# Optimization experiments

Hardware: AMD Instinct MI355X
Metric: run time of the kernel (lower is better)

## Reference

```python
import jax, jax.numpy as jnp
import numpy as np
from math import log2, ceil

HEADS, DIM_HEAD, BLOCK, EPS = 16, 64, 16, 1e-8


def setup_inputs() -> dict:
    key = jax.random.key(0)
    k1, k2, k3, k4 = jax.random.split(key, 4)
    b, n, dim = 4, 4096, 1024
    inner = HEADS * DIM_HEAD
    return {
        "x": jax.random.normal(k1, (b, n, dim), jnp.float32),
        "w_qkv": jax.random.normal(k2, (inner * 3, dim), jnp.float32) * 0.02,
        "w_out": jax.random.normal(k3, (dim, inner), jnp.float32) * 0.02,
        "b_out": jax.random.normal(k4, (dim,), jnp.float32) * 0.02,
    }


def reference(x, w_qkv, w_out, b_out):
    b, n, dim = x.shape
    pad_to_len = 2 ** ceil(log2(n))
    if pad_to_len != n:
        x = jnp.pad(x, ((0, 0), (0, pad_to_len - n), (0, 0)))
    qkv = x @ w_qkv.T  # torch Linear (no bias): weight is [out, in]
    q, k, v = jnp.split(qkv, 3, axis=-1)

    def split_heads(t):
        return t.reshape(b, pad_to_len, HEADS, DIM_HEAD).transpose(0, 2, 1, 3).reshape(b * HEADS, pad_to_len, DIM_HEAD)

    q = split_heads(q) * DIM_HEAD ** -0.5
    k = split_heads(k)
    v = split_heads(v)

    num_levels = int(log2(pad_to_len // BLOCK)) - 1
    # hierarchical coarsening: q,k averaged over pairs, v summed over pairs
    qkvs = [(q, k, v)]
    for _ in range(num_levels):
        q = q.reshape(q.shape[0], -1, 2, DIM_HEAD).mean(2)
        k = k.reshape(k.shape[0], -1, 2, DIM_HEAD).mean(2)
        v = v.reshape(v.shape[0], -1, 2, DIM_HEAD).sum(2)
        qkvs.append((q, k, v))

    neg_max = -jnp.finfo(x.dtype).max
    idx = jnp.arange(pad_to_len)
    Ysum = jnp.zeros((b * HEADS, pad_to_len, DIM_HEAD), x.dtype)
    Asum = jnp.zeros((b * HEADS, pad_to_len), x.dtype)

    for lvl, (ql, kl, vl) in enumerate(qkvs):
        B = ql.shape[0]
        nb = ql.shape[1] // BLOCK  # number of blocks at this level
        ql = ql.reshape(B, nb, BLOCK, DIM_HEAD)
        kl = kl.reshape(B, nb, BLOCK, DIM_HEAD)
        vl = vl.reshape(B, nb, BLOCK, DIM_HEAD)
        if lvl == 0:
            # finest level: causal diagonal block attention
            S = jnp.einsum('bnid,bnjd->bnij', ql, kl)
            S = jnp.where(jnp.triu(jnp.ones((BLOCK, BLOCK), bool), 1), neg_max, S)
            S = S - S.max(-1, keepdims=True)
            A = jnp.exp(S)
            y = jnp.einsum('bnij,bnjd->bnid', A, vl).reshape(B, pad_to_len, DIM_HEAD)
            Av = A.sum(-1).reshape(B, pad_to_len)
        else:
            # off-diagonal: second block of each pair attends to first block of pair
            q2 = ql.reshape(B, nb // 2, 2, BLOCK, DIM_HEAD)[:, :, 1]
            k1b = kl.reshape(B, nb // 2, 2, BLOCK, DIM_HEAD)[:, :, 0]  # flip_every_two then take [:,1]
            v1b = vl.reshape(B, nb // 2, 2, BLOCK, DIM_HEAD)[:, :, 0]
            S = jnp.einsum('bnid,bnjd->bnij', q2, k1b)
            S = S - S.max(-1, keepdims=True)
            A = jnp.exp(S)
            y = jnp.einsum('bnij,bnjd->bnid', A, v1b)  # [B, nb/2, BLOCK, d]
            Av = A.sum(-1)
            # zero-pad first block of each pair, flatten blocks back to sequence
            y = jnp.pad(y[:, :, None], ((0, 0), (0, 0), (1, 0), (0, 0), (0, 0))).reshape(B, -1, DIM_HEAD)
            Av = jnp.pad(Av[:, :, None], ((0, 0), (0, 0), (1, 0), (0, 0))).reshape(B, -1)
            # expand coarsened positions to full resolution (consecutive repeats)
            y = jnp.repeat(y, 2 ** lvl, axis=1)
            Av = jnp.repeat(Av, 2 ** lvl, axis=1)
        # causal keep-mask: max original index inside the coarsened key group <= query index
        seq_key = (idx >> lvl << lvl) + (2 ** lvl - 1)
        keep = seq_key <= idx  # at lvl=0 seq_key == idx -> keep all
        Ysum = Ysum + jnp.where(keep[None, :, None], y, 0.0)
        Asum = Asum + jnp.where(keep[None, :], Av, 0.0)

    out = Ysum / (Asum + EPS)[..., None]
    out = out.reshape(b, HEADS, pad_to_len, DIM_HEAD).transpose(0, 2, 1, 3).reshape(b, pad_to_len, HEADS * DIM_HEAD)
    out = out @ w_out.T + b_out
    return out[:, :n]
```

## Files before the change

kernel.cpp:

```cpp
#include <hip/hip_runtime.h>

typedef __bf16 bf16_t;
typedef __attribute__((ext_vector_type(8))) __bf16 bf16x8;
typedef __attribute__((ext_vector_type(4))) float f32x4;

#define MFMA(a,b,c) __builtin_amdgcn_mfma_f32_16x16x32_bf16(a,b,c,0,0,0)

static __device__ __forceinline__ unsigned short f2bfbits(float f){
  unsigned int u = __builtin_bit_cast(unsigned int, f);
  return (unsigned short)((u + 0x7FFFu + ((u >> 16) & 1u)) >> 16);
}
static __device__ __forceinline__ float bits2f(unsigned int b){
  return __builtin_bit_cast(float, b << 16);
}
static __device__ __forceinline__ void gl_lds16(const void* g, void* l){
  __builtin_amdgcn_global_load_lds(
      (const __attribute__((address_space(1))) void*)(g),
      (__attribute__((address_space(3))) void*)(l), 16, 0, 0);
}
static __device__ __forceinline__ void unpack8(uint4 raw, float* f){
  f[0]=bits2f(raw.x&0xFFFFu); f[1]=bits2f(raw.x>>16);
  f[2]=bits2f(raw.y&0xFFFFu); f[3]=bits2f(raw.y>>16);
  f[4]=bits2f(raw.z&0xFFFFu); f[5]=bits2f(raw.z>>16);
  f[6]=bits2f(raw.w&0xFFFFu); f[7]=bits2f(raw.w>>16);
}

__global__ __launch_bounds__(256) void cvt_f32_bf16(const float* __restrict__ in,
                                                    unsigned short* __restrict__ out,
                                                    long n4){
  const long stride = (long)gridDim.x * 256;
  for (long i = (long)blockIdx.x * 256 + threadIdx.x; i < n4; i += stride){
    float4 v = *(const float4*)(in + i * 4);
    unsigned long long pack = (unsigned long long)f2bfbits(v.x)
      | ((unsigned long long)f2bfbits(v.y) << 16)
      | ((unsigned long long)f2bfbits(v.z) << 32)
      | ((unsigned long long)f2bfbits(v.w) << 48);
    *(unsigned long long*)(out + i * 4) = pack;
  }
}

template<int MODE>
__global__ __launch_bounds__(512, 2) void gemm256(
    const unsigned short* __restrict__ A, const unsigned short* __restrict__ B,
    const int K, const int nbx,
    unsigned short* __restrict__ oq, unsigned short* __restrict__ ok2, unsigned short* __restrict__ ov,
    float* __restrict__ outp, const float* __restrict__ bias)
{
  __shared__ char lds[131072];
  const int t = threadIdx.x;
  const int lane = t & 63, wid = t >> 6;
  const int wr = wid >> 2, wc = wid & 3;
  const int r16 = lane & 15, g = lane >> 4;

  const int nb = gridDim.x, cpx = nb >> 3;
  const int lin = (blockIdx.x & 7) * cpx + (blockIdx.x >> 3);
  const int by = lin / nbx, bx = lin - by * nbx;
  const long row0 = (long)by * 256, col0 = (long)bx * 256;

  const unsigned short* gA[4]; const unsigned short* gB[4];
  int ldsoff[4];
  #pragma unroll
  for (int r2 = 0; r2 < 4; ++r2){
    const int flat = r2*512 + t;
    const int row = flat >> 3, slot = flat & 7;
    const int slotg = slot ^ (row & 7);
    gA[r2] = A + (row0 + row) * K + slotg*8;
    gB[r2] = B + (col0 + row) * K + slotg*8;
    ldsoff[r2] = (r2*512 + wid*64) * 16;
  }

  f32x4 acc[8][4];
  #pragma unroll
  for (int m = 0; m < 8; ++m)
    #pragma unroll
    for (int n = 0; n < 4; ++n)
      acc[m][n] = (f32x4){0.f, 0.f, 0.f, 0.f};

  const int nk = K >> 6;

  #define SA(tt, r) gl_lds16(gA[r] + (tt)*64, lds + ((tt)&1)*65536 + ldsoff[r])
  #define SB(tt, r) gl_lds16(gB[r] + (tt)*64, lds + ((tt)&1)*65536 + 32768 + ldsoff[r])

  SA(0,0); SA(0,2); SB(0,0); SB(0,1); SB(0,2); SB(0,3); SA(0,1); SA(0,3);
  asm volatile("s_waitcnt vmcnt(2)" ::: "memory");
  __builtin_amdgcn_s_barrier();

  for (int kt = 0; kt < nk; ++kt){
    char* ldsA = lds + (kt & 1)*65536;
    char* ldsB = ldsA + 32768;
    const bool more = (kt + 1 < nk);
    bf16x8 bfrag[4][2];

    {
      #pragma unroll
      for (int n = 0; n < 4; ++n)
        #pragma unroll
        for (int kk = 0; kk < 2; ++kk){
          const int row = wc*64 + n*16 + r16;
          bfrag[n][kk] = *(const bf16x8*)(ldsB + row*128 + (((kk*4 + g) ^ (row & 7)) * 16));
        }
      bf16x8 afr[2][2];
      #pragma unroll
      for (int mi = 0; mi < 2; ++mi)
        #pragma unroll
        for (int kk = 0; kk < 2; ++kk){
          const int row = wr*128 + mi*16 + r16;
          afr[mi][kk] = *(const bf16x8*)(ldsA + row*128 + (((kk*4 + g) ^ (row & 7)) * 16));
        }
      if (more){ SA(kt+1,0); SA(kt+1,2); }
      __builtin_amdgcn_s_barrier();
      asm volatile("s_waitcnt lgkmcnt(0)" ::: "memory");
      __builtin_amdgcn_sched_barrier(0);
      __builtin_amdgcn_s_setprio(1);
      #pragma unroll
      for (int mi = 0; mi < 2; ++mi)
        #pragma unroll
        for (int n = 0; n < 4; ++n)
          #pragma unroll
          for (int kk = 0; kk < 2; ++kk)
            acc[mi][n] = MFMA(afr[mi][kk], bfrag[n][kk], acc[mi][n]);
      __builtin_amdgcn_s_setprio(0);
      __builtin_amdgcn_s_barrier();
    }
    {
      bf16x8 afr[2][2];
      #pragma unroll
      for (int mi = 0; mi < 2; ++mi)
        #pragma unroll
        for (int kk = 0; kk < 2; ++kk){
          const int row = wr*128 + (2+mi)*16 + r16;
          afr[mi][kk] = *(const bf16x8*)(ldsA + row*128 + (((kk*4 + g) ^ (row & 7)) * 16));
        }
      if (more){
        SB(kt+1,0); SB(kt+1,1);
        asm volatile("s_waitcnt vmcnt(4)" ::: "memory");
      } else {
        asm volatile("s_waitcnt vmcnt(0)" ::: "memory");
      }
      __builtin_amdgcn_s_barrier();
      asm volatile("s_waitcnt lgkmcnt(0)" ::: "memory");
      __builtin_amdgcn_sched_barrier(0);
      __builtin_amdgcn_s_setprio(1);
      #pragma unroll
      for (int mi = 0; mi < 2; ++mi)
        #pragma unroll
        for (int n = 0; n < 4; ++n)
          #pragma unroll
          for (int kk = 0; kk < 2; ++kk)
            acc[2+mi][n] = MFMA(afr[mi][kk], bfrag[n][kk], acc[2+mi][n]);
      __builtin_amdgcn_s_setprio(0);
      __builtin_amdgcn_s_barrier();
    }
    {
      bf16x8 afr[2][2];
      #pragma unroll
      for (int mi = 0; mi < 2; ++mi)
        #pragma unroll
        for (int kk = 0; kk < 2; ++kk){
          const int row = wr*128 + (4+mi)*16 + r16;
          afr[mi][kk] = *(const bf16x8*)(ldsA + row*128 + (((kk*4 + g) ^ (row & 7)) * 16));
        }
      if (more){ SB(kt+1,2); SB(kt+1,3); }
      __builtin_amdgcn_s_barrier();
      asm volatile("s_waitcnt lgkmcnt(0)" ::: "memory");
      __builtin_amdgcn_sched_barrier(0);
      __builtin_amdgcn_s_setprio(1);
      #pragma unroll
      for (int mi = 0; mi < 2; ++mi)
        #pragma unroll
        for (int n = 0; n < 4; ++n)
          #pragma unroll
          for (int kk = 0; kk < 2; ++kk)
            acc[4+mi][n] = MFMA(afr[mi][kk], bfrag[n][kk], acc[4+mi][n]);
      __builtin_amdgcn_s_setprio(0);
      __builtin_amdgcn_s_barrier();
    }
    {
      bf16x8 afr[2][2];
      #pragma unroll
      for (int mi = 0; mi < 2; ++mi)
        #pragma unroll
        for (int kk = 0; kk < 2; ++kk){
          const int row = wr*128 + (6+mi)*16 + r16;
          afr[mi][kk] = *(const bf16x8*)(ldsA + row*128 + (((kk*4 + g) ^ (row & 7)) * 16));
        }
      if (more){
        SA(kt+1,1); SA(kt+1,3);
        asm volatile("s_waitcnt vmcnt(2)" ::: "memory");
      }
      __builtin_amdgcn_s_barrier();
      asm volatile("s_waitcnt lgkmcnt(0)" ::: "memory");
      __builtin_amdgcn_sched_barrier(0);
      __builtin_amdgcn_s_setprio(1);
      #pragma unroll
      for (int mi = 0; mi < 2; ++mi)
        #pragma unroll
        for (int n = 0; n < 4; ++n)
          #pragma unroll
          for (int kk = 0; kk < 2; ++kk)
            acc[6+mi][n] = MFMA(afr[mi][kk], bfrag[n][kk], acc[6+mi][n]);
      __builtin_amdgcn_s_setprio(0);
      __builtin_amdgcn_s_barrier();
    }
  }
  #undef SA
  #undef SB

  if (MODE == 0){
    __syncthreads();
    const int which = (int)(col0 >> 10);
    const int h = (int)((col0 & 1023) >> 6) + wc;
    const float sc = (which == 0) ? 0.125f : 1.0f;
    unsigned short* st = (unsigned short*)lds + wid*8192;
    #pragma unroll
    for (int pass = 0; pass < 2; ++pass){
      #pragma unroll
      for (int mm = 0; mm < 4; ++mm)
        #pragma unroll
        for (int n = 0; n < 4; ++n)
          #pragma unroll
          for (int q2 = 0; q2 < 4; ++q2)
            st[(mm*16 + g*4 + q2)*72 + n*16 + r16] = f2bfbits(acc[pass*4 + mm][n][q2] * sc);
      const long prow0 = row0 + wr*128 + pass*64;
      if (which < 2){
        unsigned short* dst = (which == 0) ? oq : ok2;
        #pragma unroll
        for (int rd = 0; rd < 8; ++rd){
          const int rl = rd*8 + (lane >> 3);
          const int gr = lane & 7;
          uint4 v = *(const uint4*)&st[rl*72 + gr*8];
          const long ii = prow0 + rl;
          const int b_ = (int)(ii >> 12), pos = (int)(ii & 4095);
          *(uint4*)&dst[(((long)b_*16 + h)*4096 + pos)*64 + gr*8] = v;
        }
      } else {
        #pragma unroll
        for (int rd = 0; rd < 8; ++rd){
          const int blk = rd >> 1;
          const int d = (rd & 1)*32 + (lane >> 1);
          const int kkh = lane & 1;
          unsigned short tmp[8];
          #pragma unroll
          for (int j = 0; j < 8; ++j)
            tmp[j] = st[(blk*16 + kkh*8 + j)*72 + d];
          uint4 v;
          v.x = (unsigned int)tmp[0] | ((unsigned int)tmp[1] << 16);
          v.y = (unsigned int)tmp[2] | ((unsigned int)tmp[3] << 16);
          v.z = (unsigned int)tmp[4] | ((unsigned int)tmp[5] << 16);
          v.w = (unsigned int)tmp[6] | ((unsigned int)tmp[7] << 16);
          const long posblk = (prow0 >> 4) + blk;
          const int b_ = (int)(posblk >> 8), blkg = (int)(posblk & 255);
          *(uint4*)&ov[(((long)b_*16 + h)*256 + blkg)*1024 + d*16 + kkh*8] = v;
        }
      }
      __builtin_amdgcn_sched_barrier(0);
    }
  } else {
    #pragma unroll
    for (int n = 0; n < 4; ++n){
      const long j = col0 + wc*64 + n*16 + r16;
      const float bi = bias[j];
      #pragma unroll
      for (int m = 0; m < 8; ++m){
        const long ib = row0 + wr*128 + m*16 + g*4;
        #pragma unroll
        for (int q2 = 0; q2 < 4; ++q2)
          outp[(ib + q2)*1024 + j] = acc[m][n][q2] + bi;
      }
    }
  }
}

__global__ __launch_bounds__(256) void coarsen(
    const unsigned short* __restrict__ q0, const unsigned short* __restrict__ k0,
    const unsigned short* __restrict__ vt0,
    unsigned short* __restrict__ qch, unsigned short* __restrict__ kch,
    unsigned short* __restrict__ vch)
{
  __shared__ float Abuf[128*65];
  __shared__ float Bbuf[64*65];
  const int t = threadIdx.x;
  const int chunk = blockIdx.x;
  const int bh = blockIdx.y;
  const int arr = blockIdx.z;
  if (arr < 2){
    const unsigned short* src = (arr == 0) ? q0 : k0;
    const long sbase = ((long)bh*4096 + (long)chunk*128) * 64;
    #pragma unroll
    for (int it = 0; it < 4; ++it){
      const int idx = it*2048 + t*8;
      uint4 raw = *(const uint4*)(src + sbase + idx);
      float f[8]; unpack8(raw, f);
      const int rowb = idx >> 6, colb = idx & 63;
      #pragma unroll
      for (int j = 0; j < 8; ++j) Abuf[rowb*65 + colb + j] = f[j];
    }
  } else {
    const long sbase = ((long)bh*256 + (long)chunk*8) * 1024;
    #pragma unroll
    for (int it = 0; it < 4; ++it){
      const int flat = it*2048 + t*8;
      const int blk = flat >> 10, rem = flat & 1023;
      const int d = rem >> 4, kk0 = rem & 15;
      uint4 raw = *(const uint4*)(vt0 + sbase + flat);
      float f[8]; unpack8(raw, f);
      #pragma unroll
      for (int j = 0; j < 8; ++j) Abuf[(blk*16 + kk0 + j)*65 + d] = f[j];
    }
  }
  __syncthreads();
  float* cur = Abuf; float* nxt = Bbuf;
  int rows = 128;
  const int Spre[8] = {0, 0, 1024, 1536, 1792, 1920, 1984, 2016};
  for (int l = 1; l <= 7; ++l){
    rows >>= 1;
    const int P = 2048 >> l;
    const long base = (long)Spre[l] * 4096;
    for (int e = t; e < rows*64; e += 256){
      const int p = e >> 6, d = e & 63;
      const float a = cur[(2*p)*65 + d], b2 = cur[(2*p + 1)*65 + d];
      const float val = (arr == 2) ? (a + b2) : 0.5f*(a + b2);
      nxt[p*65 + d] = val;
      const int pl = chunk*rows + p;
      const int cb = pl >> 4, ci = cb >> 1;
      if (arr == 0){
        if (cb & 1) qch[base + ((long)bh*P + ci*16 + (pl & 15))*64 + d] = f2bfbits(val);
      } else if (arr == 1){
        if (!(cb & 1)) kch[base + ((long)bh*P + ci*16 + (pl & 15))*64 + d] = f2bfbits(val);
      } else if (rows < 16){
        if (!(cb & 1)) vch[base + (long)bh*P*64 + ci*1024 + d*16 + (pl & 15)] = f2bfbits(val);
      }
    }
    __syncthreads();
    if (arr == 2 && rows >= 16){
      const int nblk = rows >> 4;
      for (int oe = t; oe < nblk*1024; oe += 256){
        const int bl = oe >> 10, rem = oe & 1023;
        const int cb = chunk*nblk + bl;
        if (cb & 1) continue;
        const int d = rem >> 4, kk = rem & 15;
        vch[base + (long)bh*P*64 + (long)(cb>>1)*1024 + rem] = f2bfbits(nxt[(bl*16 + kk)*65 + d]);
      }
    }
    float* tmp = cur; cur = nxt; nxt = tmp;
  }
}

__global__ __launch_bounds__(256) void attn_fused(
    const unsigned short* __restrict__ q0, const unsigned short* __restrict__ k0,
    const unsigned short* __restrict__ vt0,
    const unsigned short* __restrict__ qch, const unsigned short* __restrict__ kch,
    const unsigned short* __restrict__ vch,
    unsigned short* __restrict__ ybf)
{
  const int lane = threadIdx.x & 63;
  const int w = threadIdx.x >> 6;
  const int B0 = blockIdx.x * 4 + w;
  const int bh = blockIdx.y;
  const int b_ = bh >> 4, h = bh & 15;
  const int r = lane & 15, g = lane >> 4;
  __shared__ float accs_all[4][16*64];
  __shared__ float denoms_all[4][16];
  float* accs = accs_all[w];
  float* denoms = denoms_all[w];

  {
    const long base = ((long)bh*4096 + (long)B0*16) * 64;
    const bf16x8 ka0 = *(const bf16x8*)(k0 + base + r*64 + g*8);
    const bf16x8 ka1 = *(const bf16x8*)(k0 + base + r*64 + g*8 + 32);
    const bf16x8 qb0 = *(const bf16x8*)(q0 + base + r*64 + g*8);
    const bf16x8 qb1 = *(const bf16x8*)(q0 + base + r*64 + g*8 + 32);
    f32x4 s = {0.f,0.f,0.f,0.f};
    s = MFMA(ka0, qb0, s);
    s = MFMA(ka1, qb1, s);

    float p[4];
    float mx = -3.402823466e38f;
    #pragma unroll
    for (int j = 0; j < 4; ++j){
      const int c = g*4 + j;
      p[j] = (c <= r) ? s[j] : -3.402823466e38f;
      mx = fmaxf(mx, p[j]);
    }
    mx = fmaxf(mx, __shfl_xor(mx, 16));
    mx = fmaxf(mx, __shfl_xor(mx, 32));
    float rs = 0.f;
    #pragma unroll
    for (int j = 0; j < 4; ++j){
      const int c = g*4 + j;
      p[j] = (c <= r) ? __expf(p[j] - mx) : 0.f;
      rs += p[j];
    }
    rs += __shfl_xor(rs, 16);
    rs += __shfl_xor(rs, 32);

    float x16[4], x32[4], x48[4];
    #pragma unroll
    for (int j = 0; j < 4; ++j){
      x16[j] = __shfl_xor(p[j], 16);
      x32[j] = __shfl_xor(p[j], 32);
      x48[j] = __shfl_xor(p[j], 48);
    }
    bf16x8 af;
    #pragma unroll
    for (int j = 0; j < 4; ++j){
      const float lo = (g == 0) ? p[j]   : (g == 1) ? x48[j] : 0.f;
      const float hi = (g == 0) ? x16[j] : (g == 1) ? x32[j] : 0.f;
      af[j]   = (bf16_t)lo;
      af[j+4] = (bf16_t)hi;
    }
    const unsigned short* vt = vt0 + ((long)bh*256 + B0) * 1024;
    #pragma unroll
    for (int nb = 0; nb < 4; ++nb){
      bf16x8 bv;
      #pragma unroll
      for (int j = 0; j < 8; ++j) bv[j] = (bf16_t)0.f;
      if (g < 2) bv = *(const bf16x8*)(vt + (nb*16 + r)*16 + g*8);
      f32x4 y = {0.f,0.f,0.f,0.f};
      y = MFMA(af, bv, y);
      #pragma unroll
      for (int q2 = 0; q2 < 4; ++q2)
        accs[(g*4 + q2)*64 + nb*16 + r] = y[q2];
    }
    if (g == 0) denoms[r] = rs;
  }

  const int Spre[8] = {0, 0, 1024, 1536, 1792, 1920, 1984, 2016};
  for (int l = 1; l <= 7; ++l){
    int nr, lo, cb;
    if (l <= 4){
      nr = 16 >> l;
      lo = (B0 & ((1 << l) - 1)) << (4 - l);
      cb = B0 >> l;
    } else {
      const int m = 1 << (l - 4);
      if ((B0 & (m - 1)) != m - 1) continue;
      const int qrow = ((B0 + 1) >> (l - 4)) - 1;
      cb = qrow >> 4; lo = qrow & 15; nr = 1;
    }
    if (!(cb & 1)) continue;
    const int ci = cb >> 1;
    const int P = 2048 >> l;
    const long base = (long)Spre[l] * 4096;
    const long qb_base = base + ((long)bh*P + ci*16) * 64;
    const long kv_base = base + (long)bh*P*64 + (long)ci*1024;

    const bf16x8 ka0 = *(const bf16x8*)(kch + qb_base + r*64 + g*8);
    const bf16x8 ka1 = *(const bf16x8*)(kch + qb_base + r*64 + g*8 + 32);
    const bf16x8 qb0 = *(const bf16x8*)(qch + qb_base + r*64 + g*8);
    const bf16x8 qb1 = *(const bf16x8*)(qch + qb_base + r*64 + g*8 + 32);
    f32x4 s = {0.f,0.f,0.f,0.f};
    s = MFMA(ka0, qb0, s);
    s = MFMA(ka1, qb1, s);

    float p[4];
    float mx = fmaxf(fmaxf(s[0], s[1]), fmaxf(s[2], s[3]));
    mx = fmaxf(mx, __shfl_xor(mx, 16));
    mx = fmaxf(mx, __shfl_xor(mx, 32));
    float rs = 0.f;
    #pragma unroll
    for (int j = 0; j < 4; ++j){ p[j] = __expf(s[j] - mx); rs += p[j]; }
    rs += __shfl_xor(rs, 16);
    rs += __shfl_xor(rs, 32);

    float x16[4], x32[4], x48[4];
    #pragma unroll
    for (int j = 0; j < 4; ++j){
      x16[j] = __shfl_xor(p[j], 16);
      x32[j] = __shfl_xor(p[j], 32);
      x48[j] = __shfl_xor(p[j], 48);
    }
    bf16x8 af;
    #pragma unroll
    for (int j = 0; j < 4; ++j){
      const float lo2 = (g == 0) ? p[j]   : (g == 1) ? x48[j] : 0.f;
      const float hi2 = (g == 0) ? x16[j] : (g == 1) ? x32[j] : 0.f;
      af[j]   = (bf16_t)lo2;
      af[j+4] = (bf16_t)hi2;
    }
    #pragma unroll
    for (int nb = 0; nb < 4; ++nb){
      bf16x8 bv;
      #pragma unroll
      for (int j = 0; j < 8; ++j) bv[j] = (bf16_t)0.f;
      if (g < 2) bv = *(const bf16x8*)(vch + kv_base + (nb*16 + r)*16 + g*8);
      f32x4 y = {0.f,0.f,0.f,0.f};
      y = MFMA(af, bv, y);
      #pragma unroll
      for (int q2 = 0; q2 < 4; ++q2){
        const int row = g*4 + q2;
        if (row >= lo && row < lo + nr){
          const int ii = (((cb*16 + row + 1) << l) - 1) - (B0 << 4);
          accs[ii*64 + nb*16 + r] += y[q2];
        }
      }
    }
    if (g == 0 && r >= lo && r < lo + nr){
      const int ii = (((cb*16 + r + 1) << l) - 1) - (B0 << 4);
      denoms[ii] += rs;
    }
  }

  const int row = lane >> 2, d0 = (lane & 3) * 16;
  const float inv = 1.f / (denoms[row] + 1e-8f);
  unsigned int wv[8];
  #pragma unroll
  for (int j2 = 0; j2 < 8; ++j2){
    const float a = accs[row*64 + d0 + 2*j2]      * inv;
    const float b2 = accs[row*64 + d0 + 2*j2 + 1] * inv;
    wv[j2] = (unsigned int)f2bfbits(a) | ((unsigned int)f2bfbits(b2) << 16);
  }
  uint4* dst = (uint4*)(ybf + ((long)b_*4096 + B0*16 + row)*1024 + h*64 + d0);
  dst[0] = make_uint4(wv[0], wv[1], wv[2], wv[3]);
  dst[1] = make_uint4(wv[4], wv[5], wv[6], wv[7]);
}

extern "C" void kernel_launch(void* const* d_in, const int* in_sizes, int n_in,
                              void* d_out, int out_size, void* d_ws, size_t ws_size,
                              hipStream_t stream){
  const float* x    = (const float*)d_in[0];
  const float* wqkv = (const float*)d_in[1];
  const float* wout = (const float*)d_in[2];
  const float* bout = (const float*)d_in[3];
  float* out = (float*)d_out;
  char* ws = (char*)d_ws;

  unsigned short* wqb = (unsigned short*)(ws + 0L);
  unsigned short* wob = (unsigned short*)(ws + 6291456L);
  unsigned short* xb  = (unsigned short*)(ws + 8388608L);
  unsigned short* q0  = (unsigned short*)(ws + 41943040L);
  unsigned short* k0  = (unsigned short*)(ws + 75497472L);
  unsigned short* vt0 = (unsigned short*)(ws + 109051904L);
  unsigned short* qch = (unsigned short*)(ws + 142606336L);
  unsigned short* kch = (unsigned short*)(ws + 159252480L);
  unsigned short* vch = (unsigned short*)(ws + 175898624L);
  unsigned short* ybf = xb;

  cvt_f32_bf16<<<2048, 256, 0, stream>>>(x,    xb,  (long)16384*1024/4);
  cvt_f32_bf16<<<512,  256, 0, stream>>>(wqkv, wqb, (long)3072*1024/4);
  cvt_f32_bf16<<<256,  256, 0, stream>>>(wout, wob, (long)1024*1024/4);

  gemm256<0><<<768, 512, 0, stream>>>(xb, wqb, 1024, 12, q0, k0, vt0, nullptr, nullptr);
  coarsen<<<dim3(32,64,3), 256, 0, stream>>>(q0, k0, vt0, qch, kch, vch);
  attn_fused<<<dim3(64,64), 256, 0, stream>>>(q0, k0, vt0, qch, kch, vch, ybf);
  gemm256<1><<<256, 512, 0, stream>>>(ybf, wob, 1024, 4, nullptr, nullptr, nullptr, out, bout);
}
```

Baseline: 306.6 us.

## Share coarse-level attention blocks across warps in a 64-row tile and merge convert kernels

The attention kernel now has each workgroup own a 64-row output tile with a shared accumulator. Each coarse level's block is computed once per tile and distributed across the four warps, where before every warp recomputed redundant coarse-level work for its own 16 rows. Results go into shared memory with atomicAdd between two barriers. The three fp32-to-bf16 convert launches are also merged into one kernel, which removes launch overhead at the cost of per-element branching.

Result: slower. 321.1 us (+4.7%).

```diff
diff --git a/kernel.cpp b/kernel.cpp
--- a/kernel.cpp
+++ b/kernel.cpp
@@ -25,17 +25,25 @@
   f[6]=bits2f(raw.w&0xFFFFu); f[7]=bits2f(raw.w>>16);
 }
 
-__global__ __launch_bounds__(256) void cvt_f32_bf16(const float* __restrict__ in,
-                                                    unsigned short* __restrict__ out,
-                                                    long n4){
+__global__ __launch_bounds__(256) void cvt_all(const float* __restrict__ x,
+                                               const float* __restrict__ wqkv,
+                                               const float* __restrict__ wout,
+                                               unsigned short* __restrict__ xb,
+                                               unsigned short* __restrict__ wqb,
+                                               unsigned short* __restrict__ wob){
+  const long n4 = 5242880;
   const long stride = (long)gridDim.x * 256;
   for (long i = (long)blockIdx.x * 256 + threadIdx.x; i < n4; i += stride){
-    float4 v = *(const float4*)(in + i * 4);
+    const float* in; unsigned short* out; long e;
+    if (i < 4194304){ in = x; out = xb; e = i; }
+    else if (i < 4980736){ in = wqkv; out = wqb; e = i - 4194304; }
+    else { in = wout; out = wob; e = i - 4980736; }
+    float4 v = *(const float4*)(in + e * 4);
     unsigned long long pack = (unsigned long long)f2bfbits(v.x)
       | ((unsigned long long)f2bfbits(v.y) << 16)
       | ((unsigned long long)f2bfbits(v.z) << 32)
       | ((unsigned long long)f2bfbits(v.w) << 48);
-    *(unsigned long long*)(out + i * 4) = pack;
+    *(unsigned long long*)(out + e * 4) = pack;
   }
 }
 
@@ -346,6 +354,76 @@
   }
 }
 
+static __device__ __forceinline__ void attn_level(
+    int l, int cb, int row_lo, int row_n, int bh,
+    const unsigned short* __restrict__ qch, const unsigned short* __restrict__ kch,
+    const unsigned short* __restrict__ vch,
+    float* accs, float* denoms, int lane)
+{
+  const int r = lane & 15, g = lane >> 4;
+  const int Spre[8] = {0, 0, 1024, 1536, 1792, 1920, 1984, 2016};
+  const int ci = cb >> 1;
+  const int P = 2048 >> l;
+  const long base = (long)Spre[l] * 4096;
+  const long qb_base = base + ((long)bh*P + ci*16) * 64;
+  const long kv_base = base + (long)bh*P*64 + (long)ci*1024;
+
+  const bf16x8 ka0 = *(const bf16x8*)(kch + qb_base + r*64 + g*8);
+  const bf16x8 ka1 = *(const bf16x8*)(kch + qb_base + r*64 + g*8 + 32);
+  const bf16x8 qb0 = *(const bf16x8*)(qch + qb_base + r*64 + g*8);
+  const bf16x8 qb1 = *(const bf16x8*)(qch + qb_base + r*64 + g*8 + 32);
+  f32x4 s = {0.f,0.f,0.f,0.f};
+  s = MFMA(ka0, qb0, s);
+  s = MFMA(ka1, qb1, s);
+
+  float p[4];
+  float mx = fmaxf(fmaxf(s[0], s[1]), fmaxf(s[2], s[3]));
+  mx = fmaxf(mx, __shfl_xor(mx, 16));
+  mx = fmaxf(mx, __shfl_xor(mx, 32));
+  float rs = 0.f;
+  #pragma unroll
+  for (int j = 0; j < 4; ++j){ p[j] = __expf(s[j] - mx); rs += p[j]; }
+  rs += __shfl_xor(rs, 16);
+  rs += __shfl_xor(rs, 32);
+
+  float x16[4], x32[4], x48[4];
+  #pragma unroll
+  for (int j = 0; j < 4; ++j){
+    x16[j] = __shfl_xor(p[j], 16);
+    x32[j] = __shfl_xor(p[j], 32);
+    x48[j] = __shfl_xor(p[j], 48);
+  }
+  bf16x8 af;
+  #pragma unroll
+  for (int j = 0; j < 4; ++j){
+    const float lo2 = (g == 0) ? p[j]   : (g == 1) ? x48[j] : 0.f;
+    const float hi2 = (g == 0) ? x16[j] : (g == 1) ? x32[j] : 0.f;
+    af[j]   = (bf16_t)lo2;
+    af[j+4] = (bf16_t)hi2;
+  }
+  #pragma unroll
+  for (int nb = 0; nb < 4; ++nb){
+    bf16x8 bv;
+    #pragma unroll
+    for (int j = 0; j < 8; ++j) bv[j] = (bf16_t)0.f;
+    if (g < 2) bv = *(const bf16x8*)(vch + kv_base + (nb*16 + r)*16 + g*8);
+    f32x4 y = {0.f,0.f,0.f,0.f};
+    y = MFMA(af, bv, y);
+    #pragma unroll
+    for (int q2 = 0; q2 < 4; ++q2){
+      const int row = g*4 + q2;
+      if (row >= row_lo && row < row_lo + row_n){
+        const int pos = (((cb*16 + row + 1) << l) - 1) & 63;
+        atomicAdd(&accs[pos*64 + nb*16 + r], y[q2]);
+      }
+    }
+  }
+  if (g == 0 && r >= row_lo && r < row_lo + row_n){
+    const int pos = (((cb*16 + r + 1) << l) - 1) & 63;
+    atomicAdd(&denoms[pos], rs);
+  }
+}
+
 __global__ __launch_bounds__(256) void attn_fused(
     const unsigned short* __restrict__ q0, const unsigned short* __restrict__ k0,
     const unsigned short* __restrict__ vt0,
@@ -353,18 +431,18 @@
     const unsigned short* __restrict__ vch,
     unsigned short* __restrict__ ybf)
 {
-  const int lane = threadIdx.x & 63;
-  const int w = threadIdx.x >> 6;
-  const int B0 = blockIdx.x * 4 + w;
+  const int t = threadIdx.x;
+  const int lane = t & 63;
+  const int w = t >> 6;
+  const int b = blockIdx.x;
   const int bh = blockIdx.y;
   const int b_ = bh >> 4, h = bh & 15;
   const int r = lane & 15, g = lane >> 4;
-  __shared__ float accs_all[4][16*64];
-  __shared__ float denoms_all[4][16];
-  float* accs = accs_all[w];
-  float* denoms = denoms_all[w];
+  __shared__ float accs[64*64];
+  __shared__ float denoms[64];
 
   {
+    const int B0 = b*4 + w;
     const long base = ((long)bh*4096 + (long)B0*16) * 64;
     const bf16x8 ka0 = *(const bf16x8*)(k0 + base + r*64 + g*8);
     const bf16x8 ka1 = *(const bf16x8*)(k0 + base + r*64 + g*8 + 32);
@@ -420,88 +498,28 @@
       y = MFMA(af, bv, y);
       #pragma unroll
       for (int q2 = 0; q2 < 4; ++q2)
-        accs[(g*4 + q2)*64 + nb*16 + r] = y[q2];
-    }
-    if (g == 0) denoms[r] = rs;
-  }
-
-  const int Spre[8] = {0, 0, 1024, 1536, 1792, 1920, 1984, 2016};
-  for (int l = 1; l <= 7; ++l){
-    int nr, lo, cb;
-    if (l <= 4){
-      nr = 16 >> l;
-      lo = (B0 & ((1 << l) - 1)) << (4 - l);
-      cb = B0 >> l;
-    } else {
-      const int m = 1 << (l - 4);
-      if ((B0 & (m - 1)) != m - 1) continue;
-      const int qrow = ((B0 + 1) >> (l - 4)) - 1;
-      cb = qrow >> 4; lo = qrow & 15; nr = 1;
-    }
-    if (!(cb & 1)) continue;
-    const int ci = cb >> 1;
-    const int P = 2048 >> l;
-    const long base = (long)Spre[l] * 4096;
-    const long qb_base = base + ((long)bh*P + ci*16) * 64;
-    const long kv_base = base + (long)bh*P*64 + (long)ci*1024;
-
-    const bf16x8 ka0 = *(const bf16x8*)(kch + qb_base + r*64 + g*8);
-    const bf16x8 ka1 = *(const bf16x8*)(kch + qb_base + r*64 + g*8 + 32);
-    const bf16x8 qb0 = *(const bf16x8*)(qch + qb_base + r*64 + g*8);
-    const bf16x8 qb1 = *(const bf16x8*)(qch + qb_base + r*64 + g*8 + 32);
-    f32x4 s = {0.f,0.f,0.f,0.f};
-    s = MFMA(ka0, qb0, s);
-    s = MFMA(ka1, qb1, s);
-
-    float p[4];
-    float mx = fmaxf(fmaxf(s[0], s[1]), fmaxf(s[2], s[3]));
-    mx = fmaxf(mx, __shfl_xor(mx, 16));
-    mx = fmaxf(mx, __shfl_xor(mx, 32));
-    float rs = 0.f;
-    #pragma unroll
-    for (int j = 0; j < 4; ++j){ p[j] = __expf(s[j] - mx); rs += p[j]; }
-    rs += __shfl_xor(rs, 16);
-    rs += __shfl_xor(rs, 32);
-
-    float x16[4], x32[4], x48[4];
-    #pragma unroll
-    for (int j = 0; j < 4; ++j){
-      x16[j] = __shfl_xor(p[j], 16);
-      x32[j] = __shfl_xor(p[j], 32);
-      x48[j] = __shfl_xor(p[j], 48);
-    }
-    bf16x8 af;
-    #pragma unroll
-    for (int j = 0; j < 4; ++j){
-      const float lo2 = (g == 0) ? p[j]   : (g == 1) ? x48[j] : 0.f;
-      const float hi2 = (g == 0) ? x16[j] : (g == 1) ? x32[j] : 0.f;
-      af[j]   = (bf16_t)lo2;
-      af[j+4] = (bf16_t)hi2;
-    }
-    #pragma unroll
-    for (int nb = 0; nb < 4; ++nb){
-      bf16x8 bv;
-      #pragma unroll
-      for (int j = 0; j < 8; ++j) bv[j] = (bf16_t)0.f;
-      if (g < 2) bv = *(const bf16x8*)(vch + kv_base + (nb*16 + r)*16 + g*8);
-      f32x4 y = {0.f,0.f,0.f,0.f};
-      y = MFMA(af, bv, y);
-      #pragma unroll
-      for (int q2 = 0; q2 < 4; ++q2){
-        const int row = g*4 + q2;
-        if (row >= lo && row < lo + nr){
-          const int ii = (((cb*16 + row + 1) << l) - 1) - (B0 << 4);
-          accs[ii*64 + nb*16 + r] += y[q2];
-        }
-      }
-    }
-    if (g == 0 && r >= lo && r < lo + nr){
-      const int ii = (((cb*16 + r + 1) << l) - 1) - (B0 << 4);
-      denoms[ii] += rs;
-    }
-  }
-
-  const int row = lane >> 2, d0 = (lane & 3) * 16;
+        accs[(w*16 + g*4 + q2)*64 + nb*16 + r] = y[q2];
+    }
+    if (g == 0) denoms[w*16 + r] = rs;
+  }
+  __syncthreads();
+
+  if (w == 0){
+    attn_level(1, 2*b + 1, 0, 16, bh, qch, kch, vch, accs, denoms, lane);
+    if ((b >> 3) & 1) attn_level(5, b >> 3, (2*b) & 15, 2, bh, qch, kch, vch, accs, denoms, lane);
+  } else if (w == 1){
+    if (b & 1)        attn_level(2, b, 0, 16, bh, qch, kch, vch, accs, denoms, lane);
+    if ((b >> 4) & 1) attn_level(6, b >> 4, b & 15, 1, bh, qch, kch, vch, accs, denoms, lane);
+  } else if (w == 2){
+    if (b & 2)        attn_level(3, b >> 1, 8*(b & 1), 8, bh, qch, kch, vch, accs, denoms, lane);
+    if ((b & 1) && (((b - 1) >> 5) & 1))
+                      attn_level(7, (b - 1) >> 5, ((b - 1) >> 1) & 15, 1, bh, qch, kch, vch, accs, denoms, lane);
+  } else {
+    if (b & 4)        attn_level(4, b >> 2, 4*(b & 3), 4, bh, qch, kch, vch, accs, denoms, lane);
+  }
+  __syncthreads();
+
+  const int row = t >> 2, d0 = (t & 3) * 16;
   const float inv = 1.f / (denoms[row] + 1e-8f);
   unsigned int wv[8];
   #pragma unroll
@@ -510,7 +528,7 @@
     const float b2 = accs[row*64 + d0 + 2*j2 + 1] * inv;
     wv[j2] = (unsigned int)f2bfbits(a) | ((unsigned int)f2bfbits(b2) << 16);
   }
-  uint4* dst = (uint4*)(ybf + ((long)b_*4096 + B0*16 + row)*1024 + h*64 + d0);
+  uint4* dst = (uint4*)(ybf + ((long)b_*4096 + b*64 + row)*1024 + h*64 + d0);
   dst[0] = make_uint4(wv[0], wv[1], wv[2], wv[3]);
   dst[1] = make_uint4(wv[4], wv[5], wv[6], wv[7]);
 }
@@ -536,9 +554,7 @@
   unsigned short* vch = (unsigned short*)(ws + 175898624L);
   unsigned short* ybf = xb;
 
-  cvt_f32_bf16<<<2048, 256, 0, stream>>>(x,    xb,  (long)16384*1024/4);
-  cvt_f32_bf16<<<512,  256, 0, stream>>>(wqkv, wqb, (long)3072*1024/4);
-  cvt_f32_bf16<<<256,  256, 0, stream>>>(wout, wob, (long)1024*1024/4);
+  cvt_all<<<2048, 256, 0, stream>>>(x, wqkv, wout, xb, wqb, wob);
 
   gemm256<0><<<768, 512, 0, stream>>>(xb, wqb, 1024, 12, q0, k0, vt0, nullptr, nullptr);
   coarsen<<<dim3(32,64,3), 256, 0, stream>>>(q0, k0, vt0, qch, kch, vch);
```
